# Kernel tuning notes

Hardware: AMD Instinct MI355X
Metric: run time of the kernel (lower is better)

The kernel has to match this reference:

```python
import jax, jax.numpy as jnp
import numpy as np

N_HEAD = 16
ROPE_BASE = 10000.0


def apply_rope(x):
    # x: [B, T, H, D], torchtune interleaved-pair RoPE
    B, T, H, D = x.shape
    pos = jnp.arange(T, dtype=jnp.float32)
    freqs = 1.0 / (ROPE_BASE ** (jnp.arange(0, D, 2, dtype=jnp.float32) / D))  # [D/2]
    theta = pos[:, None] * freqs[None, :]            # [T, D/2]
    cos = jnp.cos(theta)[None, :, None, :]           # [1, T, 1, D/2]
    sin = jnp.sin(theta)[None, :, None, :]
    xp = x.reshape(B, T, H, D // 2, 2)
    x0, x1 = xp[..., 0], xp[..., 1]
    out = jnp.stack([x0 * cos - x1 * sin, x1 * cos + x0 * sin], axis=-1)
    return out.reshape(B, T, H, D).astype(x.dtype)


def setup_inputs() -> dict:
    key = jax.random.key(0)
    k1, k2, k3 = jax.random.split(key, 3)
    B, T, C = 4, 2048, 1024
    x = jax.random.normal(k1, (B, T, C), dtype=jnp.float32)
    w_qkv = jax.random.normal(k2, (C, 3 * C), dtype=jnp.float32) * 0.02
    b_qkv = jnp.zeros((3 * C,), dtype=jnp.float32)
    w_proj = jax.random.normal(k3, (C, C), dtype=jnp.float32) * 0.02
    b_proj = jnp.zeros((C,), dtype=jnp.float32)
    return {"x": x, "w_qkv": w_qkv, "b_qkv": b_qkv, "w_proj": w_proj, "b_proj": b_proj}


def reference(x, w_qkv, b_qkv, w_proj, b_proj):
    B, T, C = x.shape
    H = N_HEAD
    D = C // H
    qkv = x @ w_qkv + b_qkv                          # [B, T, 3C]
    q, k, v = jnp.split(qkv, 3, axis=-1)
    q = apply_rope(q.reshape(B, T, H, D))
    k = apply_rope(k.reshape(B, T, H, D))
    v = v.reshape(B, T, H, D)
    scale = 1.0 / jnp.sqrt(jnp.asarray(D, dtype=x.dtype))
    attn = jnp.einsum('bthd,bshd->bhts', q, k) * scale  # [B, H, T, T] (non-causal)
    attn = jax.nn.softmax(attn, axis=-1)
    out = jnp.einsum('bhts,bshd->bthd', attn, v).reshape(B, T, C)
    return out @ w_proj + b_proj
```

## Files before the change

### kernel.cpp

```cpp
#include <hip/hip_runtime.h>

typedef unsigned short ushort_t;
typedef unsigned int   uint_t;
typedef __attribute__((ext_vector_type(8))) short bf16x8;
typedef __attribute__((ext_vector_type(4))) float f32x4;

__device__ __forceinline__ ushort_t f2bf(float f) {
    union { float f; uint_t i; } x; x.f = f;
    uint_t i = x.i + 0x7fffu + ((x.i >> 16) & 1u);
    return (ushort_t)(i >> 16);
}
__device__ __forceinline__ uint_t fbits(float f) {
    union { float f; uint_t i; } x; x.f = f;
    return x.i;
}
__device__ __forceinline__ void async16(const void* g, void* l) {
    __builtin_amdgcn_global_load_lds(
        (const __attribute__((address_space(1))) uint_t*)g,
        (__attribute__((address_space(3))) uint_t*)l, 16, 0, 0);
}

__global__ __launch_bounds__(256) void conv_bf16(
    const float* __restrict__ in, ushort_t* __restrict__ outp)
{
    int i = (blockIdx.x * 256 + threadIdx.x) * 4;
    float4 v = *(const float4*)(in + i);
    uint_t a = (uint_t)f2bf(v.x) | ((uint_t)f2bf(v.y) << 16);
    uint_t b = (uint_t)f2bf(v.z) | ((uint_t)f2bf(v.w) << 16);
    uint2 st = { a, b };
    *(uint2*)(outp + i) = st;
}

__global__ __launch_bounds__(256) void transpose_conv(
    const float* __restrict__ in, ushort_t* __restrict__ outp, int R, int C)
{
    __shared__ ushort_t t[64][65];
    int r0 = blockIdx.y * 64, c0 = blockIdx.x * 64;
    int lr = threadIdx.x >> 4, lc = (threadIdx.x & 15) * 4;
#pragma unroll
    for (int rr = 0; rr < 4; ++rr) {
        float4 v = *(const float4*)(in + (size_t)(r0 + rr * 16 + lr) * C + c0 + lc);
        t[lc + 0][rr * 16 + lr] = f2bf(v.x);
        t[lc + 1][rr * 16 + lr] = f2bf(v.y);
        t[lc + 2][rr * 16 + lr] = f2bf(v.z);
        t[lc + 3][rr * 16 + lr] = f2bf(v.w);
    }
    __syncthreads();
    int oc = threadIdx.x >> 2, och = (threadIdx.x & 3) * 16;
    union { uint4 v[2]; ushort_t u[16]; } pk;
#pragma unroll
    for (int j = 0; j < 16; ++j) pk.u[j] = t[oc][och + j];
    uint4* dst = (uint4*)(outp + (size_t)(c0 + oc) * R + r0 + och);
    dst[0] = pk.v[0]; dst[1] = pk.v[1];
}

__global__ __launch_bounds__(256) void rope_table_k(float2* __restrict__ tab)
{
    int idx = blockIdx.x * 256 + threadIdx.x;
    int t = idx >> 5, i = idx & 31;
    float freq = powf(10000.0f, -(float)i * (1.0f / 32.0f));
    float sn, cs;
    sincosf((float)t * freq, &sn, &cs);
    tab[idx] = make_float2(cs, sn);
}

template <int MODE>
__global__ __launch_bounds__(256) void gemm_mfma(
    const ushort_t* __restrict__ A, const ushort_t* __restrict__ Bt,
    const float* __restrict__ bias, void* __restrict__ Cv,
    const float2* __restrict__ tab, int M, int N, int K, int coloff)
{
    __shared__ ushort_t As[128][64];
    __shared__ ushort_t Bs[128][64];
    const int tid = threadIdx.x;
    const int w = tid >> 6, lane = tid & 63, ln = lane & 15, quad = lane >> 4;
    const int wm = w >> 1, wn = w & 1;

    const int lin = blockIdx.y * gridDim.x + blockIdx.x;
    const int per = (gridDim.x * gridDim.y) >> 3;
    const int nid = (lin & 7) * per + (lin >> 3);
    const int bx = nid % gridDim.x, by = nid / gridDim.x;
    const int row0 = by * 128, col0 = bx * 128 + coloff;

    f32x4 acc[4][4] = {};

    const int swch = (lane & 7) ^ (lane >> 3);
    const ushort_t* ga = A  + (size_t)(row0 + w * 8 + (lane >> 3)) * K + swch * 8;
    const ushort_t* gb = Bt + (size_t)(col0 + w * 8 + (lane >> 3)) * K + swch * 8;
    ushort_t* la = &As[w * 8][0];
    ushort_t* lb = &Bs[w * 8][0];
    const int rch0 = ln & 7;

    for (int k0 = 0; k0 < K; k0 += 64) {
#pragma unroll
        for (int j = 0; j < 4; ++j) {
            async16(ga + (size_t)(j * 32) * K + k0, la + j * 32 * 64);
            async16(gb + (size_t)(j * 32) * K + k0, lb + j * 32 * 64);
        }
        __syncthreads();
#pragma unroll
        for (int kk = 0; kk < 2; ++kk) {
            int ch = ((kk * 4 + quad) ^ rch0) * 8;
            bf16x8 af[4], bfv[4];
#pragma unroll
            for (int mt = 0; mt < 4; ++mt)
                af[mt] = *(const bf16x8*)&As[wm * 64 + mt * 16 + ln][ch];
#pragma unroll
            for (int nt = 0; nt < 4; ++nt)
                bfv[nt] = *(const bf16x8*)&Bs[wn * 64 + nt * 16 + ln][ch];
#pragma unroll
            for (int mt = 0; mt < 4; ++mt)
#pragma unroll
                for (int nt = 0; nt < 4; ++nt) {
                    if (MODE == 2)
                        acc[mt][nt] = __builtin_amdgcn_mfma_f32_16x16x32_bf16(
                            af[mt], bfv[nt], acc[mt][nt], 0, 0, 0);
                    else
                        acc[mt][nt] = __builtin_amdgcn_mfma_f32_16x16x32_bf16(
                            bfv[nt], af[mt], acc[mt][nt], 0, 0, 0);
                }
        }
        __syncthreads();
    }

    if (MODE == 2) {
#pragma unroll
        for (int nt = 0; nt < 4; ++nt) {
            int c = col0 + wn * 64 + nt * 16 + ln;
            float bv = bias[c];
            int c2 = c - 2048;
            size_t vrow = ((size_t)(c2 >> 6)) * 64 + (c2 & 63);
#pragma unroll
            for (int mt = 0; mt < 4; ++mt) {
                int rr = row0 + wm * 64 + mt * 16 + quad * 4;
                int b = rr >> 11, t0 = rr & 2047;
                uint2 st;
                st.x = (uint_t)f2bf(acc[mt][nt][0] + bv)
                     | ((uint_t)f2bf(acc[mt][nt][1] + bv) << 16);
                st.y = (uint_t)f2bf(acc[mt][nt][2] + bv)
                     | ((uint_t)f2bf(acc[mt][nt][3] + bv) << 16);
                *(uint2*)((ushort_t*)Cv + ((size_t)b * 16 * 64 + vrow) * 2048 + t0) = st;
            }
        }
    } else {
#pragma unroll
        for (int mt = 0; mt < 4; ++mt) {
            int rr = row0 + wm * 64 + mt * 16 + ln;
#pragma unroll
            for (int nt = 0; nt < 4; ++nt) {
                int c0 = col0 + wn * 64 + nt * 16 + quad * 4;
                float4 bv = *(const float4*)(bias + c0);
                float v0 = acc[mt][nt][0] + bv.x, v1 = acc[mt][nt][1] + bv.y;
                float v2 = acc[mt][nt][2] + bv.z, v3 = acc[mt][nt][3] + bv.w;
                if (MODE == 1) {
                    int i0 = (c0 & 63) >> 1;
                    const float2* trow = tab + (size_t)(rr & 2047) * 32;
                    float2 cs0 = trow[i0], cs1 = trow[i0 + 1];
                    float o0 = v0 * cs0.x - v1 * cs0.y;
                    float o1 = v1 * cs0.x + v0 * cs0.y;
                    float o2 = v2 * cs1.x - v3 * cs1.y;
                    float o3 = v3 * cs1.x + v2 * cs1.y;
                    uint2 st;
                    st.x = (uint_t)f2bf(o0) | ((uint_t)f2bf(o1) << 16);
                    st.y = (uint_t)f2bf(o2) | ((uint_t)f2bf(o3) << 16);
                    *(uint2*)((ushort_t*)Cv + (size_t)rr * N + c0) = st;
                } else {
                    float4 st = { v0, v1, v2, v3 };
                    *(float4*)((float*)Cv + (size_t)rr * N + c0) = st;
                }
            }
        }
    }
}

__global__ __launch_bounds__(512, 2) void gemm256_rope(
    const ushort_t* __restrict__ A, const ushort_t* __restrict__ Bt,
    const float* __restrict__ bias, ushort_t* __restrict__ C,
    const float2* __restrict__ tab)
{
    __shared__ ushort_t As[2][256][64];
    __shared__ ushort_t Bs[2][256][64];

    const int tid = threadIdx.x;
    const int w = tid >> 6, lane = tid & 63, ln = lane & 15, quad = lane >> 4;
    const int wm = w >> 2, wn = w & 3;

    const int lin = blockIdx.y * 8 + blockIdx.x;
    const int nid = (lin & 7) * 32 + (lin >> 3);
    const int bx = nid & 7, by = nid >> 3;
    const int row0 = by * 256, col0 = bx * 256;

    const int r6 = tid >> 3, c8 = tid & 7;
    const int swch = c8 ^ (r6 & 7);
    const ushort_t* ga = A  + (size_t)(row0 + r6) * 1024 + swch * 8;
    const ushort_t* gb = Bt + (size_t)(col0 + r6) * 1024 + swch * 8;
    ushort_t* lau = &As[0][0][0] + tid * 8;
    ushort_t* lbu = &Bs[0][0][0] + tid * 8;
    const int rch0 = ln & 7;

    f32x4 acc[8][4] = {};

#pragma unroll
    for (int j = 0; j < 4; ++j) {
        async16(ga + (size_t)(j * 64) * 1024, lau + j * 4096);
        async16(gb + (size_t)(j * 64) * 1024, lbu + j * 4096);
    }
    asm volatile("s_waitcnt vmcnt(0)" ::: "memory");
    __builtin_amdgcn_s_barrier();

#pragma unroll 2
    for (int k = 0; k < 16; ++k) {
        const int cur = k & 1;
        const int kn = (k < 15) ? k + 1 : k;
        const size_t koff = (size_t)kn * 64;
#pragma unroll
        for (int j = 0; j < 4; ++j) {
            async16(ga + (size_t)(j * 64) * 1024 + koff, lau + (cur ^ 1) * 16384 + j * 4096);
            async16(gb + (size_t)(j * 64) * 1024 + koff, lbu + (cur ^ 1) * 16384 + j * 4096);
        }
        bf16x8 bf[4];
#pragma unroll
        for (int q = 0; q < 4; ++q) {
            const int kk = q >> 1, mh = q & 1;
            const int ch = ((kk * 4 + quad) ^ rch0) * 8;
            if (mh == 0) {
#pragma unroll
                for (int nt = 0; nt < 4; ++nt)
                    bf[nt] = *(const bf16x8*)&Bs[cur][wn * 64 + nt * 16 + ln][ch];
            }
            bf16x8 af[4];
#pragma unroll
            for (int mt = 0; mt < 4; ++mt)
                af[mt] = *(const bf16x8*)&As[cur][mh * 128 + wm * 64 + mt * 16 + ln][ch];
            __builtin_amdgcn_s_setprio(1);
#pragma unroll
            for (int mt = 0; mt < 4; ++mt)
#pragma unroll
                for (int nt = 0; nt < 4; ++nt)
                    acc[mh * 4 + mt][nt] = __builtin_amdgcn_mfma_f32_16x16x32_bf16(
                        bf[nt], af[mt], acc[mh * 4 + mt][nt], 0, 0, 0);
            __builtin_amdgcn_s_setprio(0);
            if (q == 3)
                asm volatile("s_waitcnt vmcnt(0)" ::: "memory");
            __builtin_amdgcn_s_barrier();
        }
    }

#pragma unroll
    for (int mg = 0; mg < 8; ++mg) {
        const int rr = row0 + (mg >> 2) * 128 + wm * 64 + (mg & 3) * 16 + ln;
        const float2* trow = tab + (size_t)(rr & 2047) * 32;
#pragma unroll
        for (int nt = 0; nt < 4; ++nt) {
            const int c0 = col0 + wn * 64 + nt * 16 + quad * 4;
            float4 bv = *(const float4*)(bias + c0);
            float v0 = acc[mg][nt][0] + bv.x, v1 = acc[mg][nt][1] + bv.y;
            float v2 = acc[mg][nt][2] + bv.z, v3 = acc[mg][nt][3] + bv.w;
            const int i0 = (c0 & 63) >> 1;
            float2 cs0 = trow[i0], cs1 = trow[i0 + 1];
            float o0 = v0 * cs0.x - v1 * cs0.y;
            float o1 = v1 * cs0.x + v0 * cs0.y;
            float o2 = v2 * cs1.x - v3 * cs1.y;
            float o3 = v3 * cs1.x + v2 * cs1.y;
            uint2 st;
            st.x = (uint_t)f2bf(o0) | ((uint_t)f2bf(o1) << 16);
            st.y = (uint_t)f2bf(o2) | ((uint_t)f2bf(o3) << 16);
            *(uint2*)(C + (size_t)rr * 3072 + c0) = st;
        }
    }
}

__global__ __launch_bounds__(512, 4) void attn_mfma(
    const ushort_t* __restrict__ qkv, const ushort_t* __restrict__ vtg,
    ushort_t* __restrict__ outp)
{
    __shared__ ushort_t Ks[2][64][64];
    __shared__ ushort_t Vts[2][64][64];
    __shared__ ushort_t Ps[8][16][72];

    const int tid = threadIdx.x;
    const int w = tid >> 6, lane = tid & 63, ln = lane & 15, quad = lane >> 4;
    const int bh = blockIdx.x, qt = blockIdx.y, b = bh >> 4, h = bh & 15;
    const size_t base = (size_t)b * 2048 * 3072 + h * 64;

    bf16x8 af[2][2];
#pragma unroll
    for (int s = 0; s < 2; ++s)
#pragma unroll
        for (int kk = 0; kk < 2; ++kk)
            af[s][kk] = *(const bf16x8*)(qkv + base
                + (size_t)(qt * 256 + w * 32 + s * 16 + ln) * 3072 + kk * 32 + quad * 8);

    bf16x8 ones;
#pragma unroll
    for (int j = 0; j < 8; ++j) ones[j] = (short)0x3F80;

    f32x4 oaccT[2][4] = {};
    f32x4 oneacc[2] = {};
    const float SC = 0.125f * 1.44269504f;

    const int swch = (lane & 7) ^ (lane >> 3);
    const ushort_t* kg = qkv + base + 1024 + (size_t)(lane >> 3) * 3072 + swch * 8;
    const ushort_t* vg = vtg + ((size_t)bh * 64 + (lane >> 3)) * 2048 + swch * 8;
    const int rch0 = ln & 7;
    const int r8 = w * 8;

    async16(kg + (size_t)r8 * 3072, &Ks[0][r8][0]);
    async16(vg + (size_t)r8 * 2048, &Vts[0][r8][0]);
    asm volatile("s_waitcnt vmcnt(0)" ::: "memory");
    __builtin_amdgcn_s_barrier();

    int cur = 0;
    for (int kt = 0; kt < 32; ++kt) {
        if (kt < 31) {
            async16(kg + (size_t)((kt + 1) * 64 + r8) * 3072, &Ks[cur ^ 1][r8][0]);
            async16(vg + (size_t)r8 * 2048 + (kt + 1) * 64, &Vts[cur ^ 1][r8][0]);
        }

        bf16x8 kf[2][4], vf[2][4];
#pragma unroll
        for (int kk = 0; kk < 2; ++kk) {
            int ch = ((kk * 4 + quad) ^ rch0) * 8;
#pragma unroll
            for (int nt = 0; nt < 4; ++nt) {
                kf[kk][nt] = *(const bf16x8*)&Ks[cur][nt * 16 + ln][ch];
                vf[kk][nt] = *(const bf16x8*)&Vts[cur][nt * 16 + ln][ch];
            }
        }

#pragma unroll
        for (int s = 0; s < 2; ++s) {
            f32x4 sacc[4] = {};
#pragma unroll
            for (int kk = 0; kk < 2; ++kk)
#pragma unroll
                for (int nt = 0; nt < 4; ++nt)
                    sacc[nt] = __builtin_amdgcn_mfma_f32_16x16x32_bf16(
                        kf[kk][nt], af[s][kk], sacc[nt], 0, 0, 0);

            if (s == 1)
                asm volatile("s_waitcnt lgkmcnt(0)" ::: "memory");
#pragma unroll
            for (int nt = 0; nt < 4; ++nt) {
                float e0 = __builtin_amdgcn_exp2f(fmaf(sacc[nt][0], SC, -24.0f));
                float e1 = __builtin_amdgcn_exp2f(fmaf(sacc[nt][1], SC, -24.0f));
                float e2 = __builtin_amdgcn_exp2f(fmaf(sacc[nt][2], SC, -24.0f));
                float e3 = __builtin_amdgcn_exp2f(fmaf(sacc[nt][3], SC, -24.0f));
                uint2 pk;
                pk.x = __builtin_amdgcn_perm(fbits(e1), fbits(e0), 0x07060302u);
                pk.y = __builtin_amdgcn_perm(fbits(e3), fbits(e2), 0x07060302u);
                *(uint2*)&Ps[w][ln][nt * 16 + quad * 4] = pk;
            }
            asm volatile("s_waitcnt lgkmcnt(0)" ::: "memory");

#pragma unroll
            for (int kk = 0; kk < 2; ++kk) {
                bf16x8 pf = *(const bf16x8*)&Ps[w][ln][kk * 32 + quad * 8];
                oneacc[s] = __builtin_amdgcn_mfma_f32_16x16x32_bf16(
                    ones, pf, oneacc[s], 0, 0, 0);
#pragma unroll
                for (int nt = 0; nt < 4; ++nt)
                    oaccT[s][nt] = __builtin_amdgcn_mfma_f32_16x16x32_bf16(
                        vf[kk][nt], pf, oaccT[s][nt], 0, 0, 0);
            }
        }

        asm volatile("s_waitcnt vmcnt(0) lgkmcnt(0)" ::: "memory");
        __builtin_amdgcn_s_barrier();
        cur ^= 1;
    }

#pragma unroll
    for (int s = 0; s < 2; ++s) {
        float linv = 1.0f / oneacc[s][0];
        size_t row = (size_t)b * 2048 + qt * 256 + w * 32 + s * 16 + ln;
#pragma unroll
        for (int nt = 0; nt < 4; ++nt) {
            uint2 st;
            st.x = (uint_t)f2bf(oaccT[s][nt][0] * linv)
                 | ((uint_t)f2bf(oaccT[s][nt][1] * linv) << 16);
            st.y = (uint_t)f2bf(oaccT[s][nt][2] * linv)
                 | ((uint_t)f2bf(oaccT[s][nt][3] * linv) << 16);
            *(uint2*)(outp + row * 1024 + h * 64 + nt * 16 + quad * 4) = st;
        }
    }
}

extern "C" void kernel_launch(void* const* d_in, const int* in_sizes, int n_in,
                              void* d_out, int out_size, void* d_ws, size_t ws_size,
                              hipStream_t stream)
{
    (void)in_sizes; (void)n_in; (void)out_size; (void)ws_size;

    const float* x      = (const float*)d_in[0];
    const float* w_qkv  = (const float*)d_in[1];
    const float* b_qkv  = (const float*)d_in[2];
    const float* w_proj = (const float*)d_in[3];
    const float* b_proj = (const float*)d_in[4];
    float*       out    = (float*)d_out;

    ushort_t* x_bf    = (ushort_t*)d_ws;
    ushort_t* wqkvT   = x_bf    + (size_t)8192 * 1024;
    ushort_t* wprojT  = wqkvT   + (size_t)3072 * 1024;
    ushort_t* qkv_bf  = wprojT  + (size_t)1024 * 1024;
    ushort_t* attn_bf = qkv_bf  + (size_t)8192 * 3072;
    ushort_t* vtg     = attn_bf + (size_t)8192 * 1024;
    float2*   tab     = (float2*)(vtg + (size_t)64 * 64 * 2048);

    conv_bf16<<<8192, 256, 0, stream>>>(x, x_bf);
    transpose_conv<<<dim3(48, 16), 256, 0, stream>>>(w_qkv, wqkvT, 1024, 3072);
    transpose_conv<<<dim3(16, 16), 256, 0, stream>>>(w_proj, wprojT, 1024, 1024);
    rope_table_k<<<256, 256, 0, stream>>>(tab);

    gemm256_rope<<<dim3(8, 32), 512, 0, stream>>>(x_bf, wqkvT, b_qkv, qkv_bf, tab);

    gemm_mfma<2><<<dim3(8, 64), 256, 0, stream>>>(
        x_bf, wqkvT, b_qkv, vtg, nullptr, 8192, 3072, 1024, 2048);

    attn_mfma<<<dim3(64, 8), 512, 0, stream>>>(qkv_bf, vtg, attn_bf);

    gemm_mfma<0><<<dim3(8, 64), 256, 0, stream>>>(
        attn_bf, wprojT, b_proj, out, nullptr, 8192, 1024, 1024, 0);
}
```

Baseline: 279.9 us.

## Triple-buffer QKV GEMM K-loop with 32-wide K tiles and prefetch depth two

Reworks the shared-memory pipeline of the fused QKV GEMM+RoPE kernel from two 64-wide K stages to three 32-wide K stages. Loads are issued two iterations ahead with partial vmcnt waits, and there is now one barrier per 32-wide K step instead of four per 64-wide step. The XOR swizzle is changed to match the narrower 32-column rows. The aim is to hide global-load latency behind MFMA work and cut barrier overhead. In exchange there are twice as many outer iterations, and the loop is no longer unrolled, which may add loop overhead.

```diff
diff --git a/kernel.cpp b/kernel.cpp
--- a/kernel.cpp
+++ b/kernel.cpp
@@ -178,8 +178,8 @@
     const float* __restrict__ bias, ushort_t* __restrict__ C,
     const float2* __restrict__ tab)
 {
-    __shared__ ushort_t As[2][256][64];
-    __shared__ ushort_t Bs[2][256][64];
+    __shared__ ushort_t As[3][256][32];
+    __shared__ ushort_t Bs[3][256][32];
 
     const int tid = threadIdx.x;
     const int w = tid >> 6, lane = tid & 63, ln = lane & 15, quad = lane >> 4;
@@ -190,44 +190,46 @@
     const int bx = nid & 7, by = nid >> 3;
     const int row0 = by * 256, col0 = bx * 256;
 
-    const int r6 = tid >> 3, c8 = tid & 7;
-    const int swch = c8 ^ (r6 & 7);
-    const ushort_t* ga = A  + (size_t)(row0 + r6) * 1024 + swch * 8;
-    const ushort_t* gb = Bt + (size_t)(col0 + r6) * 1024 + swch * 8;
+    const int r4 = tid >> 2, c4 = tid & 3;
+    const int key_w = (r4 & 3) ^ ((r4 >> 2) & 3);
+    const int sc = c4 ^ key_w;
+    const ushort_t* gA0 = A  + (size_t)(row0 + r4)       * 1024 + sc * 8;
+    const ushort_t* gA1 = A  + (size_t)(row0 + r4 + 128) * 1024 + sc * 8;
+    const ushort_t* gB0 = Bt + (size_t)(col0 + r4)       * 1024 + sc * 8;
+    const ushort_t* gB1 = Bt + (size_t)(col0 + r4 + 128) * 1024 + sc * 8;
     ushort_t* lau = &As[0][0][0] + tid * 8;
     ushort_t* lbu = &Bs[0][0][0] + tid * 8;
-    const int rch0 = ln & 7;
-
+
+    const int key_r = (ln & 3) ^ (ln >> 2);
     f32x4 acc[8][4] = {};
 
 #pragma unroll
-    for (int j = 0; j < 4; ++j) {
-        async16(ga + (size_t)(j * 64) * 1024, lau + j * 4096);
-        async16(gb + (size_t)(j * 64) * 1024, lbu + j * 4096);
-    }
-    asm volatile("s_waitcnt vmcnt(0)" ::: "memory");
+    for (int t = 0; t < 2; ++t) {
+        const size_t ko = (size_t)t * 32;
+        async16(gA0 + ko, lau + t * 8192 + 0 * 4096);
+        async16(gA1 + ko, lau + t * 8192 + 1 * 4096);
+        async16(gB0 + ko, lbu + t * 8192 + 0 * 4096);
+        async16(gB1 + ko, lbu + t * 8192 + 1 * 4096);
+    }
+    asm volatile("s_waitcnt vmcnt(4)" ::: "memory");
     __builtin_amdgcn_s_barrier();
 
-#pragma unroll 2
-    for (int k = 0; k < 16; ++k) {
-        const int cur = k & 1;
-        const int kn = (k < 15) ? k + 1 : k;
-        const size_t koff = (size_t)kn * 64;
-#pragma unroll
-        for (int j = 0; j < 4; ++j) {
-            async16(ga + (size_t)(j * 64) * 1024 + koff, lau + (cur ^ 1) * 16384 + j * 4096);
-            async16(gb + (size_t)(j * 64) * 1024 + koff, lbu + (cur ^ 1) * 16384 + j * 4096);
-        }
+    int cur = 0, nb = 2;
+    for (int k = 0; k < 32; ++k) {
+        if (k < 30) {
+            const size_t ko = (size_t)(k + 2) * 32;
+            async16(gA0 + ko, lau + nb * 8192 + 0 * 4096);
+            async16(gA1 + ko, lau + nb * 8192 + 1 * 4096);
+            async16(gB0 + ko, lbu + nb * 8192 + 0 * 4096);
+            async16(gB1 + ko, lbu + nb * 8192 + 1 * 4096);
+        }
+        const int ch = ((quad ^ key_r) & 3) * 8;
         bf16x8 bf[4];
 #pragma unroll
-        for (int q = 0; q < 4; ++q) {
-            const int kk = q >> 1, mh = q & 1;
-            const int ch = ((kk * 4 + quad) ^ rch0) * 8;
-            if (mh == 0) {
-#pragma unroll
-                for (int nt = 0; nt < 4; ++nt)
-                    bf[nt] = *(const bf16x8*)&Bs[cur][wn * 64 + nt * 16 + ln][ch];
-            }
+        for (int nt = 0; nt < 4; ++nt)
+            bf[nt] = *(const bf16x8*)&Bs[cur][wn * 64 + nt * 16 + ln][ch];
+#pragma unroll
+        for (int mh = 0; mh < 2; ++mh) {
             bf16x8 af[4];
 #pragma unroll
             for (int mt = 0; mt < 4; ++mt)
@@ -240,10 +242,12 @@
                     acc[mh * 4 + mt][nt] = __builtin_amdgcn_mfma_f32_16x16x32_bf16(
                         bf[nt], af[mt], acc[mh * 4 + mt][nt], 0, 0, 0);
             __builtin_amdgcn_s_setprio(0);
-            if (q == 3)
-                asm volatile("s_waitcnt vmcnt(0)" ::: "memory");
-            __builtin_amdgcn_s_barrier();
-        }
+        }
+        if (k < 30) asm volatile("s_waitcnt vmcnt(4) lgkmcnt(0)" ::: "memory");
+        else        asm volatile("s_waitcnt vmcnt(0) lgkmcnt(0)" ::: "memory");
+        __builtin_amdgcn_s_barrier();
+        cur = (cur == 2) ? 0 : cur + 1;
+        nb  = (nb  == 2) ? 0 : nb  + 1;
     }
 
 #pragma unroll
```

After: 287.8 us. 1.03x slower.
